# Kernel optimization log

Hardware: AMD Instinct MI355X
Metric: run time of the kernel (lower is better)

Reference implementation:

```python
import jax, jax.numpy as jnp
import numpy as np

# Module hyper-parameters (eval mode: remove_rand_on_eval=True => no random additional points)
B, H, C, E = 2, 8, 2048, 1024
D = 64          # head_size
KP = 8          # k (points per query per head)
P = 2 * KP      # num_points = k * 2**rank, rank = 1


def setup_inputs() -> dict:
    key = jax.random.key(0)
    ks = jax.random.split(key, 10)
    x = jax.random.normal(ks[0], (B, C, E), jnp.float32)
    attention_mask = jnp.ones((B, C), jnp.int32)  # accepted but unused, as in the torch forward
    # hyper() outputs (abstract in the class): continuous means in [0, C-1), positive sigmas, values
    means = jax.random.uniform(ks[1], (B, H, C, KP, 1), jnp.float32) * (C - 1)
    sigmas = jax.random.uniform(ks[2], (B, H, C, KP), jnp.float32) * 2.0 + 0.5
    values = jax.random.normal(ks[3], (B, H, C, KP), jnp.float32)
    s_in = 1.0 / np.sqrt(E).astype(np.float32)
    s_u = 1.0 / np.sqrt(H * D).astype(np.float32)
    Wk = jax.random.normal(ks[4], (E, H * D), jnp.float32) * s_in
    Wq = jax.random.normal(ks[5], (E, H * D), jnp.float32) * s_in
    Wv = jax.random.normal(ks[6], (E, H * D), jnp.float32) * s_in
    Wu = jax.random.normal(ks[7], (H * D, E), jnp.float32) * s_u
    bu = jnp.zeros((E,), jnp.float32)
    return dict(x=x, attention_mask=attention_mask, means=means, sigmas=sigmas,
                values=values, Wk=Wk, Wq=Wq, Wv=Wv, Wu=Wu, bu=bu)


def reference(x, attention_mask, means, sigmas, values, Wk, Wq, Wv, Wu, bu):
    b, c, e = x.shape
    h, d, kp, p = H, D, KP, P

    # ---- ngenerate (eval: only the 2**rank = 2 integer corners per mean, clamped in-range) ----
    m = means[..., 0]                                  # (b,h,c,k)
    i0 = jnp.clip(jnp.floor(m).astype(jnp.int32), 0, c - 1)
    i1 = jnp.clip(i0 + 1, 0, c - 1)
    idx = jnp.stack([i0, i1], axis=-1).reshape(b, h, c, p)   # (b,h,c,P)
    idx_fl = idx.astype(jnp.float32)

    # ---- densities: unnormalized Gaussian of each integer point under each of the k means ----
    diff = idx_fl[..., :, None] - m[..., None, :]            # (b,h,c,P,k)
    dens = jnp.exp(-0.5 * (diff / sigmas[..., None, :]) ** 2)

    # ---- nduplicates: zero densities of repeated index tuples (keep first occurrence) ----
    eq = idx[..., :, None] == idx[..., None, :]              # (b,h,c,P,P)
    earlier = jnp.tril(jnp.ones((p, p), bool), k=-1)         # q < p
    dup = jnp.any(eq & earlier, axis=-1)                     # (b,h,c,P)
    dens = jnp.where(dup[..., None], 0.0, dens)

    # normalize over dim=2 (context), exactly as the torch code does
    dens = dens / (dens.sum(axis=2, keepdims=True) + 1e-8)

    # density-weighted continuous values -> per-point weights
    weights = (values[..., None, :] * dens).sum(axis=-1)     # (b,h,c,P)

    # ---- projections ----
    inv_sqrt_d = 1.0 / np.sqrt(d).astype(np.float32)
    Kt = (x @ Wk).reshape(b, c, h, d).transpose(0, 2, 1, 3) * inv_sqrt_d  # (b,h,c,d)
    Qt = (x @ Wq).reshape(b, c, h, d).transpose(0, 2, 1, 3) * inv_sqrt_d
    Vt = (x @ Wv).reshape(b, c, h, d).transpose(0, 2, 1, 3)

    # ---- gather K/V at the sparse indices ----
    flat = idx.reshape(b, h, c * p, 1)
    Kg = jnp.take_along_axis(Kt, flat, axis=2).reshape(b, h, c, p, d)
    Vg = jnp.take_along_axis(Vt, flat, axis=2).reshape(b, h, c, p, d)

    dots = jnp.einsum('bhcd,bhcpd->bhcp', Qt, Kg)
    new_weights = jax.nn.softmax(weights * dots, axis=-1)    # (b,h,c,P)

    head_reps = jnp.einsum('bhcpd,bhcp->bhcd', Vg, new_weights)
    united = head_reps.transpose(0, 2, 1, 3).reshape(b, c, h * d)
    new_out = united @ Wu + bu

    # ---- scatter-add sparse weights into dense attention matrix ----
    bi = jnp.arange(b)[:, None, None, None]
    hi = jnp.arange(h)[None, :, None, None]
    ci = jnp.arange(c)[None, None, :, None]
    attentions = jnp.zeros((b, h, c, c), jnp.float32).at[bi, hi, ci, idx].add(new_weights)

    return new_out, attentions
```

## Files before the change

### kernel.cpp

```cpp
#include <hip/hip_runtime.h>
#include <math.h>
#include <stdint.h>

#define B_ 2
#define H_ 8
#define C_ 2048
#define E_ 1024
#define D_ 64
#define KP_ 8
#define P_ 16
#define HD_ 512
#define ROWS_ 32768
#define M_ 4096

typedef __bf16 bf16x8 __attribute__((ext_vector_type(8)));
typedef float f32x4 __attribute__((ext_vector_type(4)));
typedef uint16_t u16x8 __attribute__((ext_vector_type(8)));

__device__ inline uint16_t f2bf(float f) {
    union { float f; uint32_t u; } v; v.f = f;
    uint32_t u = v.u + 0x7FFF + ((v.u >> 16) & 1);
    return (uint16_t)(u >> 16);
}
__device__ inline float bf2f(uint16_t h) {
    union { uint32_t u; float f; } v; v.u = ((uint32_t)h) << 16;
    return v.f;
}

__device__ inline void gload16(const uint16_t* g, uint16_t* l) {
    __builtin_amdgcn_global_load_lds(
        (const __attribute__((address_space(1))) void*)g,
        (__attribute__((address_space(3))) void*)l, 16, 0, 0);
}

__global__ __launch_bounds__(256) void prep_kernel(
    const float* __restrict__ x,
    const float* __restrict__ Wq, const float* __restrict__ Wk,
    const float* __restrict__ Wv, const float* __restrict__ Wu,
    const float* __restrict__ means, const float* __restrict__ sigmas,
    uint16_t* __restrict__ xb, uint16_t* __restrict__ Wall,
    uint16_t* __restrict__ Wut, float* __restrict__ S)
{
    const int bx = blockIdx.x;
    if (bx < 2048) {
        const int i = (bx * 256 + threadIdx.x) * 8;
        const float4 a = *(const float4*)(x + i);
        const float4 b = *(const float4*)(x + i + 4);
        u16x8 o;
        o[0] = f2bf(a.x); o[1] = f2bf(a.y); o[2] = f2bf(a.z); o[3] = f2bf(a.w);
        o[4] = f2bf(b.x); o[5] = f2bf(b.y); o[6] = f2bf(b.z); o[7] = f2bf(b.w);
        *(u16x8*)(xb + i) = o;
        return;
    }
    if (bx < 4096) {
        const int t = bx - 2048;
        const int z = t >> 9;
        const float* in; uint16_t* out; int R, Cc; float scale;
        if (z == 0)      { in = Wq; out = Wall;               R = E_;  Cc = HD_; scale = 0.125f; }
        else if (z == 1) { in = Wk; out = Wall + 512 * 1024;  R = E_;  Cc = HD_; scale = 0.125f; }
        else if (z == 2) { in = Wv; out = Wall + 1024 * 1024; R = E_;  Cc = HD_; scale = 1.0f; }
        else             { in = Wu; out = Wut;                R = HD_; Cc = E_;  scale = 1.0f; }
        const int tiles_x = Cc >> 5;
        const int ti = t & 511;
        const int tx = ti % tiles_x;
        const int ty = ti / tiles_x;
        const int r0 = ty * 32, c0 = tx * 32;
        __shared__ float tbuf[32][33];
        const int lx = threadIdx.x & 31, ly = threadIdx.x >> 5;
#pragma unroll
        for (int i = 0; i < 4; ++i)
            tbuf[ly * 4 + i][lx] = in[(size_t)(r0 + ly * 4 + i) * Cc + c0 + lx];
        __syncthreads();
#pragma unroll
        for (int i = 0; i < 4; ++i)
            out[(size_t)(c0 + ly * 4 + i) * R + r0 + lx] =
                f2bf(tbuf[lx][ly * 4 + i] * scale);
        return;
    }
    const int row = (bx - 4096) * 256 + threadIdx.x;
    const int lane = threadIdx.x & 63;
    const int bh = row >> 11;

    __shared__ float Sacc[128];
    if (threadIdx.x < 128) Sacc[threadIdx.x] = 0.0f;
    __syncthreads();

    const float* mrow = means + (size_t)row * 8;
    const float* srow = sigmas + (size_t)row * 8;
    const float4 ma = *(const float4*)(mrow);
    const float4 mb = *(const float4*)(mrow + 4);
    const float4 sa = *(const float4*)(srow);
    const float4 sb = *(const float4*)(srow + 4);
    const float mm[8] = {ma.x, ma.y, ma.z, ma.w, mb.x, mb.y, mb.z, mb.w};
    const float sg[8] = {sa.x, sa.y, sa.z, sa.w, sb.x, sb.y, sb.z, sb.w};

    int idx[16];
#pragma unroll
    for (int j = 0; j < 8; ++j) {
        int i0 = (int)floorf(mm[j]);
        i0 = min(max(i0, 0), C_ - 1);
        idx[2 * j] = i0;
        idx[2 * j + 1] = min(i0 + 1, C_ - 1);
    }
    unsigned dupm = 0;
#pragma unroll
    for (int p = 1; p < 16; ++p) {
        bool d = false;
#pragma unroll
        for (int q = 0; q < 15; ++q)
            if (q < p) d = d || (idx[q] == idx[p]);
        if (d) dupm |= (1u << p);
    }

    const int rev = ((lane & 1) << 5) | ((lane & 2) << 3) | ((lane & 4) << 1) |
                    ((lane & 8) >> 1) | ((lane & 16) >> 3) | ((lane & 32) >> 5);

#pragma unroll
    for (int ph = 0; ph < 2; ++ph) {
        float a[64];
#pragma unroll
        for (int j = 0; j < 64; ++j) {
            const int p = ph * 8 + (j >> 3);
            const int kk = j & 7;
            const float fi = (float)idx[p];
            const float t = (fi - mm[kk]) / sg[kk];
            const float e = expf(-0.5f * t * t);
            a[j] = ((dupm >> p) & 1u) ? 0.0f : e;
        }
#pragma unroll
        for (int b = 0; b < 6; ++b) {
            const int n = 32 >> b;
            const bool hi = (lane >> b) & 1;
#pragma unroll
            for (int j = 0; j < n; ++j) {
                float send = hi ? a[j] : a[j + n];
                float recv = __shfl_xor(send, 1 << b);
                a[j] = (hi ? a[j + n] : a[j]) + recv;
            }
        }
        atomicAdd(&Sacc[ph * 64 + rev], a[0]);
    }
    __syncthreads();
    if (threadIdx.x < 128)
        atomicAdd(&S[bh * 128 + threadIdx.x], Sacc[threadIdx.x]);
}

__global__ __launch_bounds__(256) void gemm_qkv_kernel(
    const uint16_t* __restrict__ xb, const uint16_t* __restrict__ Wall,
    uint16_t* __restrict__ Qt, uint16_t* __restrict__ Kt,
    uint16_t* __restrict__ Vt)
{
    const int K = E_;
    const int m0 = blockIdx.y * 128;
    const int n0 = blockIdx.x * 64;
    const int z = n0 >> 9;
    uint16_t* __restrict__ Out = (z == 0) ? Qt : (z == 1) ? Kt : Vt;
    const int h = (n0 & 511) >> 6;

    __shared__ __align__(16) uint16_t smem[24576];

    const int tid = threadIdx.x;
    const int w = tid >> 6, lane = tid & 63;

    f32x4 acc[2][4] = {};

    const uint16_t* gP[3];
    uint16_t* lP[3];
#pragma unroll
    for (int j = 0; j < 3; ++j) {
        const int ci = w * 3 + j;
        const int rr = (ci & 7) * 16 + (lane >> 2);
        const int ko = (lane & 3) * 8;
        if (ci < 8) {
            gP[j] = xb + (size_t)(m0 + rr) * K + ko;
            lP[j] = &smem[ci * 512];
        } else {
            const int cb = ci - 8;
            gP[j] = Wall + (size_t)(n0 + cb * 16 + (lane >> 2)) * K + ko;
            lP[j] = &smem[4096 + cb * 512];
        }
    }

    const int fr = lane & 15;
    const int fk = (lane >> 4) * 8;

    auto stage = [&](int buf, int k0) {
        const int off = buf * 12288;
#pragma unroll
        for (int j = 0; j < 3; ++j) {
            gload16(gP[j] + k0,      lP[j] + off);
            gload16(gP[j] + k0 + 32, lP[j] + off + 6144);
        }
    };

    stage(0, 0);
    __syncthreads();
    int cur = 0;
    for (int k0 = 0; k0 < K; k0 += 64) {
        if (k0 + 64 < K) stage(cur ^ 1, k0 + 64);
        const int off = cur * 12288;
#pragma unroll
        for (int half = 0; half < 2; ++half) {
            const int base = off + half * 6144;
            bf16x8 af[2], bf[4];
#pragma unroll
            for (int mt = 0; mt < 2; ++mt)
                af[mt] = *(const bf16x8*)&smem[base + (w * 32 + mt * 16 + fr) * 32 + fk];
#pragma unroll
            for (int nt = 0; nt < 4; ++nt)
                bf[nt] = *(const bf16x8*)&smem[base + 4096 + (nt * 16 + fr) * 32 + fk];
#pragma unroll
            for (int mt = 0; mt < 2; ++mt)
#pragma unroll
                for (int nt = 0; nt < 4; ++nt)
                    acc[mt][nt] = __builtin_amdgcn_mfma_f32_16x16x32_bf16(
                        af[mt], bf[nt], acc[mt][nt], 0, 0, 0);
        }
        __syncthreads();
        cur ^= 1;
    }

#pragma unroll
    for (int mt = 0; mt < 2; ++mt)
#pragma unroll
        for (int nt = 0; nt < 4; ++nt) {
            const int col = nt * 16 + fr;
#pragma unroll
            for (int r = 0; r < 4; ++r) {
                const int rw = w * 32 + mt * 16 + (lane >> 4) * 4 + r;
                smem[rw * 72 + col] = f2bf(acc[mt][nt][r]);
            }
        }
    __syncthreads();
#pragma unroll
    for (int it = 0; it < 4; ++it) {
        const int j = it * 256 + tid;
        const int row = j >> 3, c8 = (j & 7) * 8;
        const int m = m0 + row;
        const int b = m >> 11, c = m & (C_ - 1);
        *(u16x8*)&Out[(((size_t)(b * H_ + h) * C_ + c) << 6) + c8] =
            *(const u16x8*)&smem[row * 72 + c8];
    }
}

__global__ __launch_bounds__(256) void gemm_out_kernel(
    const uint16_t* __restrict__ U, const uint16_t* __restrict__ Wut,
    const float* __restrict__ bu, float* __restrict__ out)
{
    const int K = HD_;
    const int m0 = blockIdx.y * 128;
    const int n0 = blockIdx.x * 64;

    __shared__ __align__(16) uint16_t smem[24576];

    const int tid = threadIdx.x;
    const int w = tid >> 6, lane = tid & 63;

    f32x4 acc[2][4] = {};

    const uint16_t* gP[3];
    uint16_t* lP[3];
#pragma unroll
    for (int j = 0; j < 3; ++j) {
        const int ci = w * 3 + j;
        const int ko = (lane & 3) * 8;
        if (ci < 8) {
            gP[j] = U + (size_t)(m0 + ci * 16 + (lane >> 2)) * K + ko;
            lP[j] = &smem[ci * 512];
        } else {
            const int cb = ci - 8;
            gP[j] = Wut + (size_t)(n0 + cb * 16 + (lane >> 2)) * K + ko;
            lP[j] = &smem[4096 + cb * 512];
        }
    }

    const int fr = lane & 15;
    const int fk = (lane >> 4) * 8;

    auto stage = [&](int buf, int k0) {
        const int off = buf * 12288;
#pragma unroll
        for (int j = 0; j < 3; ++j) {
            gload16(gP[j] + k0,      lP[j] + off);
            gload16(gP[j] + k0 + 32, lP[j] + off + 6144);
        }
    };

    stage(0, 0);
    __syncthreads();
    int cur = 0;
    for (int k0 = 0; k0 < K; k0 += 64) {
        if (k0 + 64 < K) stage(cur ^ 1, k0 + 64);
        const int off = cur * 12288;
#pragma unroll
        for (int half = 0; half < 2; ++half) {
            const int base = off + half * 6144;
            bf16x8 af[2], bf[4];
#pragma unroll
            for (int mt = 0; mt < 2; ++mt)
                af[mt] = *(const bf16x8*)&smem[base + (w * 32 + mt * 16 + fr) * 32 + fk];
#pragma unroll
            for (int nt = 0; nt < 4; ++nt)
                bf[nt] = *(const bf16x8*)&smem[base + 4096 + (nt * 16 + fr) * 32 + fk];
#pragma unroll
            for (int mt = 0; mt < 2; ++mt)
#pragma unroll
                for (int nt = 0; nt < 4; ++nt)
                    acc[mt][nt] = __builtin_amdgcn_mfma_f32_16x16x32_bf16(
                        af[mt], bf[nt], acc[mt][nt], 0, 0, 0);
        }
        __syncthreads();
        cur ^= 1;
    }

#pragma unroll
    for (int mt = 0; mt < 2; ++mt) {
#pragma unroll
        for (int nt = 0; nt < 4; ++nt) {
            const int n = n0 + nt * 16 + fr;
            const float bias = bu[n];
#pragma unroll
            for (int r = 0; r < 4; ++r) {
                const int m = m0 + w * 32 + mt * 16 + (lane >> 4) * 4 + r;
                out[(size_t)m * E_ + n] = acc[mt][nt][r] + bias;
            }
        }
    }
}

__global__ __launch_bounds__(256) void attn_kernel(
    const float* __restrict__ means, const float* __restrict__ sigmas,
    const float* __restrict__ values, const float* __restrict__ S,
    const uint16_t* __restrict__ Qt, const uint16_t* __restrict__ Kt,
    const uint16_t* __restrict__ Vt, uint16_t* __restrict__ united,
    float* __restrict__ attn)
{
    __shared__ float rowbuf[4][2048];
    const int w = threadIdx.x >> 6;
    const int lane = threadIdx.x & 63;
    const int bid = blockIdx.x;
    const int swz = (bid & 7) * 1024 + (bid >> 3);
    const int row = swz * 4 + w;
    const int bh = row >> 11;
    const int c = row & (C_ - 1);
    const int b = bh >> 3;
    const int h = bh & 7;

    const float* mrow = means + (size_t)row * 8;
    const float4 ma = *(const float4*)(mrow);
    const float4 mb = *(const float4*)(mrow + 4);
    const float mm[8] = {ma.x, ma.y, ma.z, ma.w, mb.x, mb.y, mb.z, mb.w};

    int idx[16];
#pragma unroll
    for (int j = 0; j < 8; ++j) {
        int i0 = (int)floorf(mm[j]);
        i0 = min(max(i0, 0), C_ - 1);
        idx[2 * j] = i0;
        idx[2 * j + 1] = min(i0 + 1, C_ - 1);
    }

    const int p = lane >> 2, g = lane & 3;
    int kidx = 0;
#pragma unroll
    for (int q = 0; q < 16; ++q)
        if (q == p) kidx = idx[q];

    const uint16_t* Qrow = Qt + ((size_t)row << 6);
    const uint16_t* Krow = Kt + ((((size_t)bh << 11) + kidx) << 6);
    const u16x8 qa = *(const u16x8*)(Qrow + g * 16);
    const u16x8 qb = *(const u16x8*)(Qrow + g * 16 + 8);
    const u16x8 ka = *(const u16x8*)(Krow + g * 16);
    const u16x8 kb = *(const u16x8*)(Krow + g * 16 + 8);
    const uint16_t* Vbh = Vt + ((size_t)bh << 17);
    uint16_t vv[16];
#pragma unroll
    for (int q = 0; q < 16; ++q)
        vv[q] = Vbh[((size_t)idx[q] << 6) + lane];

    bool dup = false;
#pragma unroll
    for (int q = 0; q < 15; ++q)
        dup = dup || ((q < p) && (idx[q] == kidx));

    float mA = 0.f, mB = 0.f;
#pragma unroll
    for (int q = 0; q < 4; ++q)
        if (q == g) { mA = mm[q]; mB = mm[q + 4]; }
    const float* srow = sigmas + (size_t)row * 8;
    const float* vrow = values + (size_t)row * 8;
    const float* Sp = S + bh * 128 + p * 8;
    const float sgA = srow[g], sgB = srow[g + 4];
    const float vlA = vrow[g], vlB = vrow[g + 4];
    const float SvA = Sp[g],   SvB = Sp[g + 4];
    const float fi = (float)kidx;
    const float tA = (fi - mA) / sgA;
    const float tB = (fi - mB) / sgB;
    const float eA = expf(-0.5f * tA * tA);
    const float eB = expf(-0.5f * tB * tB);
    float wp = dup ? 0.0f
                   : fmaf(vlA, eA / (SvA + 1e-8f), vlB * eB / (SvB + 1e-8f));
    wp += __shfl_xor(wp, 1);
    wp += __shfl_xor(wp, 2);

    float dot = 0.0f;
#pragma unroll
    for (int j = 0; j < 8; ++j) {
        dot = fmaf(bf2f(qa[j]), bf2f(ka[j]), dot);
        dot = fmaf(bf2f(qb[j]), bf2f(kb[j]), dot);
    }
    dot += __shfl_xor(dot, 1);
    dot += __shfl_xor(dot, 2);

    const float logit = wp * dot;

    float mx = logit;
#pragma unroll
    for (int off = 4; off < 64; off <<= 1)
        mx = fmaxf(mx, __shfl_xor(mx, off));
    const float e = expf(logit - mx);
    float se = e;
#pragma unroll
    for (int off = 4; off < 64; off <<= 1)
        se += __shfl_xor(se, off);
    const float sm = e / se;

    float smv[16];
#pragma unroll
    for (int q = 0; q < 16; ++q)
        smv[q] = __shfl(sm, q * 4);

    float acc = 0.0f;
#pragma unroll
    for (int q = 0; q < 16; ++q)
        acc = fmaf(bf2f(vv[q]), smv[q], acc);
    united[((size_t)(b * C_ + c)) * HD_ + h * 64 + lane] = f2bf(acc);

    const f32x4 z4 = {0.f, 0.f, 0.f, 0.f};
#pragma unroll
    for (int j = 0; j < 8; ++j)
        *(f32x4*)&rowbuf[w][(j * 64 + lane) * 4] = z4;
    __syncthreads();
    if (g == 0) atomicAdd(&rowbuf[w][kidx], sm);
    __syncthreads();
    float* arow = attn + ((size_t)row << 11);
#pragma unroll
    for (int j = 0; j < 8; ++j) {
        const int o = (j * 64 + lane) * 4;
        __builtin_nontemporal_store(*(const f32x4*)&rowbuf[w][o], (f32x4*)&arow[o]);
    }
}

extern "C" void kernel_launch(void* const* d_in, const int* in_sizes, int n_in,
                              void* d_out, int out_size, void* d_ws,
                              size_t ws_size, hipStream_t stream) {
    const float* x      = (const float*)d_in[0];
    const float* means  = (const float*)d_in[2];
    const float* sigmas = (const float*)d_in[3];
    const float* values = (const float*)d_in[4];
    const float* Wk     = (const float*)d_in[5];
    const float* Wq     = (const float*)d_in[6];
    const float* Wv     = (const float*)d_in[7];
    const float* Wu     = (const float*)d_in[8];
    const float* bu     = (const float*)d_in[9];

    float* out  = (float*)d_out;
    float* attn = out + (size_t)M_ * E_;

    uint16_t* wsp = (uint16_t*)d_ws;
    uint16_t* xb     = wsp;
    uint16_t* Wall   = xb + 4194304;
    uint16_t* Wut    = Wall + 1572864;
    uint16_t* Qt     = Wut + 524288;
    uint16_t* Kt     = Qt + 2097152;
    uint16_t* Vt     = Kt + 2097152;
    uint16_t* united = Vt + 2097152;
    float*    S      = (float*)(united + 2097152);

    (void)hipMemsetAsync(S, 0, 2048 * sizeof(float), stream);

    prep_kernel<<<4224, 256, 0, stream>>>(
        x, Wq, Wk, Wv, Wu, means, sigmas, xb, Wall, Wut, S);
    gemm_qkv_kernel<<<dim3(24, 32), 256, 0, stream>>>(xb, Wall, Qt, Kt, Vt);
    attn_kernel<<<ROWS_ / 4, 256, 0, stream>>>(
        means, sigmas, values, S, Qt, Kt, Vt, united, attn);
    gemm_out_kernel<<<dim3(16, 32), 256, 0, stream>>>(united, Wut, bu, out);
}
```

Measured before the change: 379.5 us.

## Enlarge GEMM tiles to 128x128 with 2x2 wave layout and K-step 32

Both bf16 MFMA GEMMs (QKV projection and output projection) move from 128x64 block tiles to 128x128 tiles. Each wave now computes a 64x64 quadrant, so every A/B fragment loaded from LDS feeds more MFMAs, and each block stages half-as-many K columns per iteration (32 instead of 64). The grid shrinks by half: 384 blocks for QKV and 256 for the output GEMM. That raises per-block reuse but gives fewer blocks than the GPU's compute units, leaves more loop iterations and barriers, and raises register pressure.

```diff
diff --git a/kernel.cpp b/kernel.cpp
--- a/kernel.cpp
+++ b/kernel.cpp
@@ -152,32 +152,32 @@
 {
     const int K = E_;
     const int m0 = blockIdx.y * 128;
-    const int n0 = blockIdx.x * 64;
+    const int n0 = blockIdx.x * 128;
     const int z = n0 >> 9;
     uint16_t* __restrict__ Out = (z == 0) ? Qt : (z == 1) ? Kt : Vt;
-    const int h = (n0 & 511) >> 6;
-
-    __shared__ __align__(16) uint16_t smem[24576];
+    const int hb = (n0 & 511) >> 6;
+
+    __shared__ __align__(16) uint16_t smem[18432];
 
     const int tid = threadIdx.x;
     const int w = tid >> 6, lane = tid & 63;
-
-    f32x4 acc[2][4] = {};
-
-    const uint16_t* gP[3];
-    uint16_t* lP[3];
-#pragma unroll
-    for (int j = 0; j < 3; ++j) {
-        const int ci = w * 3 + j;
+    const int qr = w >> 1, qc = w & 1;
+
+    f32x4 acc[4][4] = {};
+
+    const uint16_t* gP[4];
+    uint16_t* lP[4];
+#pragma unroll
+    for (int j = 0; j < 4; ++j) {
+        const int ci = w * 4 + j;
         const int rr = (ci & 7) * 16 + (lane >> 2);
         const int ko = (lane & 3) * 8;
         if (ci < 8) {
             gP[j] = xb + (size_t)(m0 + rr) * K + ko;
             lP[j] = &smem[ci * 512];
         } else {
-            const int cb = ci - 8;
-            gP[j] = Wall + (size_t)(n0 + cb * 16 + (lane >> 2)) * K + ko;
-            lP[j] = &smem[4096 + cb * 512];
+            gP[j] = Wall + (size_t)(n0 + rr) * K + ko;
+            lP[j] = &smem[4096 + (ci - 8) * 512];
         }
     }
 
@@ -185,61 +185,56 @@
     const int fk = (lane >> 4) * 8;
 
     auto stage = [&](int buf, int k0) {
-        const int off = buf * 12288;
-#pragma unroll
-        for (int j = 0; j < 3; ++j) {
-            gload16(gP[j] + k0,      lP[j] + off);
-            gload16(gP[j] + k0 + 32, lP[j] + off + 6144);
-        }
+        const int off = buf * 8192;
+#pragma unroll
+        for (int j = 0; j < 4; ++j)
+            gload16(gP[j] + k0, lP[j] + off);
     };
 
     stage(0, 0);
     __syncthreads();
     int cur = 0;
-    for (int k0 = 0; k0 < K; k0 += 64) {
-        if (k0 + 64 < K) stage(cur ^ 1, k0 + 64);
-        const int off = cur * 12288;
-#pragma unroll
-        for (int half = 0; half < 2; ++half) {
-            const int base = off + half * 6144;
-            bf16x8 af[2], bf[4];
-#pragma unroll
-            for (int mt = 0; mt < 2; ++mt)
-                af[mt] = *(const bf16x8*)&smem[base + (w * 32 + mt * 16 + fr) * 32 + fk];
+    for (int k0 = 0; k0 < K; k0 += 32) {
+        if (k0 + 32 < K) stage(cur ^ 1, k0 + 32);
+        const int off = cur * 8192;
+        bf16x8 af[4], bf[4];
+#pragma unroll
+        for (int mt = 0; mt < 4; ++mt)
+            af[mt] = *(const bf16x8*)&smem[off + (qr * 64 + mt * 16 + fr) * 32 + fk];
+#pragma unroll
+        for (int nt = 0; nt < 4; ++nt)
+            bf[nt] = *(const bf16x8*)&smem[off + 4096 + (qc * 64 + nt * 16 + fr) * 32 + fk];
+#pragma unroll
+        for (int mt = 0; mt < 4; ++mt)
 #pragma unroll
             for (int nt = 0; nt < 4; ++nt)
-                bf[nt] = *(const bf16x8*)&smem[base + 4096 + (nt * 16 + fr) * 32 + fk];
-#pragma unroll
-            for (int mt = 0; mt < 2; ++mt)
-#pragma unroll
-                for (int nt = 0; nt < 4; ++nt)
-                    acc[mt][nt] = __builtin_amdgcn_mfma_f32_16x16x32_bf16(
-                        af[mt], bf[nt], acc[mt][nt], 0, 0, 0);
-        }
+                acc[mt][nt] = __builtin_amdgcn_mfma_f32_16x16x32_bf16(
+                    af[mt], bf[nt], acc[mt][nt], 0, 0, 0);
         __syncthreads();
         cur ^= 1;
     }
 
 #pragma unroll
-    for (int mt = 0; mt < 2; ++mt)
+    for (int mt = 0; mt < 4; ++mt)
 #pragma unroll
         for (int nt = 0; nt < 4; ++nt) {
-            const int col = nt * 16 + fr;
+            const int col = qc * 64 + nt * 16 + fr;
 #pragma unroll
             for (int r = 0; r < 4; ++r) {
-                const int rw = w * 32 + mt * 16 + (lane >> 4) * 4 + r;
-                smem[rw * 72 + col] = f2bf(acc[mt][nt][r]);
+                const int rw = qr * 64 + mt * 16 + (lane >> 4) * 4 + r;
+                smem[rw * 144 + col] = f2bf(acc[mt][nt][r]);
             }
         }
     __syncthreads();
 #pragma unroll
-    for (int it = 0; it < 4; ++it) {
+    for (int it = 0; it < 8; ++it) {
         const int j = it * 256 + tid;
-        const int row = j >> 3, c8 = (j & 7) * 8;
+        const int row = j >> 4, c8 = (j & 15) * 8;
         const int m = m0 + row;
         const int b = m >> 11, c = m & (C_ - 1);
-        *(u16x8*)&Out[(((size_t)(b * H_ + h) * C_ + c) << 6) + c8] =
-            *(const u16x8*)&smem[row * 72 + c8];
+        const int h = hb + (c8 >> 6);
+        *(u16x8*)&Out[(((size_t)(b * H_ + h) * C_ + c) << 6) + (c8 & 63)] =
+            *(const u16x8*)&smem[row * 144 + c8];
     }
 }
 
@@ -249,28 +244,29 @@
 {
     const int K = HD_;
     const int m0 = blockIdx.y * 128;
-    const int n0 = blockIdx.x * 64;
-
-    __shared__ __align__(16) uint16_t smem[24576];
+    const int n0 = blockIdx.x * 128;
+
+    __shared__ __align__(16) uint16_t smem[16384];
 
     const int tid = threadIdx.x;
     const int w = tid >> 6, lane = tid & 63;
-
-    f32x4 acc[2][4] = {};
-
-    const uint16_t* gP[3];
-    uint16_t* lP[3];
-#pragma unroll
-    for (int j = 0; j < 3; ++j) {
-        const int ci = w * 3 + j;
+    const int qr = w >> 1, qc = w & 1;
+
+    f32x4 acc[4][4] = {};
+
+    const uint16_t* gP[4];
+    uint16_t* lP[4];
+#pragma unroll
+    for (int j = 0; j < 4; ++j) {
+        const int ci = w * 4 + j;
+        const int rr = (ci & 7) * 16 + (lane >> 2);
         const int ko = (lane & 3) * 8;
         if (ci < 8) {
-            gP[j] = U + (size_t)(m0 + ci * 16 + (lane >> 2)) * K + ko;
+            gP[j] = U + (size_t)(m0 + rr) * K + ko;
             lP[j] = &smem[ci * 512];
         } else {
-            const int cb = ci - 8;
-            gP[j] = Wut + (size_t)(n0 + cb * 16 + (lane >> 2)) * K + ko;
-            lP[j] = &smem[4096 + cb * 512];
+            gP[j] = Wut + (size_t)(n0 + rr) * K + ko;
+            lP[j] = &smem[4096 + (ci - 8) * 512];
         }
     }
 
@@ -278,50 +274,44 @@
     const int fk = (lane >> 4) * 8;
 
     auto stage = [&](int buf, int k0) {
-        const int off = buf * 12288;
-#pragma unroll
-        for (int j = 0; j < 3; ++j) {
-            gload16(gP[j] + k0,      lP[j] + off);
-            gload16(gP[j] + k0 + 32, lP[j] + off + 6144);
-        }
+        const int off = buf * 8192;
+#pragma unroll
+        for (int j = 0; j < 4; ++j)
+            gload16(gP[j] + k0, lP[j] + off);
     };
 
     stage(0, 0);
     __syncthreads();
     int cur = 0;
-    for (int k0 = 0; k0 < K; k0 += 64) {
-        if (k0 + 64 < K) stage(cur ^ 1, k0 + 64);
-        const int off = cur * 12288;
-#pragma unroll
-        for (int half = 0; half < 2; ++half) {
-            const int base = off + half * 6144;
-            bf16x8 af[2], bf[4];
-#pragma unroll
-            for (int mt = 0; mt < 2; ++mt)
-                af[mt] = *(const bf16x8*)&smem[base + (w * 32 + mt * 16 + fr) * 32 + fk];
+    for (int k0 = 0; k0 < K; k0 += 32) {
+        if (k0 + 32 < K) stage(cur ^ 1, k0 + 32);
+        const int off = cur * 8192;
+        bf16x8 af[4], bf[4];
+#pragma unroll
+        for (int mt = 0; mt < 4; ++mt)
+            af[mt] = *(const bf16x8*)&smem[off + (qr * 64 + mt * 16 + fr) * 32 + fk];
+#pragma unroll
+        for (int nt = 0; nt < 4; ++nt)
+            bf[nt] = *(const bf16x8*)&smem[off + 4096 + (qc * 64 + nt * 16 + fr) * 32 + fk];
+#pragma unroll
+        for (int mt = 0; mt < 4; ++mt)
 #pragma unroll
             for (int nt = 0; nt < 4; ++nt)
-                bf[nt] = *(const bf16x8*)&smem[base + 4096 + (nt * 16 + fr) * 32 + fk];
-#pragma unroll
-            for (int mt = 0; mt < 2; ++mt)
-#pragma unroll
-                for (int nt = 0; nt < 4; ++nt)
-                    acc[mt][nt] = __builtin_amdgcn_mfma_f32_16x16x32_bf16(
-                        af[mt], bf[nt], acc[mt][nt], 0, 0, 0);
-        }
+                acc[mt][nt] = __builtin_amdgcn_mfma_f32_16x16x32_bf16(
+                    af[mt], bf[nt], acc[mt][nt], 0, 0, 0);
         __syncthreads();
         cur ^= 1;
     }
 
 #pragma unroll
-    for (int mt = 0; mt < 2; ++mt) {
+    for (int mt = 0; mt < 4; ++mt) {
 #pragma unroll
         for (int nt = 0; nt < 4; ++nt) {
-            const int n = n0 + nt * 16 + fr;
+            const int n = n0 + qc * 64 + nt * 16 + fr;
             const float bias = bu[n];
 #pragma unroll
             for (int r = 0; r < 4; ++r) {
-                const int m = m0 + w * 32 + mt * 16 + (lane >> 4) * 4 + r;
+                const int m = m0 + qr * 64 + mt * 16 + (lane >> 4) * 4 + r;
                 out[(size_t)m * E_ + n] = acc[mt][nt][r] + bias;
             }
         }
@@ -481,8 +471,8 @@
 
     prep_kernel<<<4224, 256, 0, stream>>>(
         x, Wq, Wk, Wv, Wu, means, sigmas, xb, Wall, Wut, S);
-    gemm_qkv_kernel<<<dim3(24, 32), 256, 0, stream>>>(xb, Wall, Qt, Kt, Vt);
+    gemm_qkv_kernel<<<dim3(12, 32), 256, 0, stream>>>(xb, Wall, Qt, Kt, Vt);
     attn_kernel<<<ROWS_ / 4, 256, 0, stream>>>(
         means, sigmas, values, S, Qt, Kt, Vt, united, attn);
-    gemm_out_kernel<<<dim3(16, 32), 256, 0, stream>>>(united, Wut, bu, out);
-}
+    gemm_out_kernel<<<dim3(8, 32), 256, 0, stream>>>(united, Wut, bu, out);
+}
```

Result: no change. 385.4 us (+1.6%).
